# Kernel tuning notes

Hardware: AMD Instinct MI355X
Metric: run time of the kernel (lower is better)

## Reference

```python
import jax, jax.numpy as jnp
import numpy as np

B, S, HID = 1, 2048, 2048
H = 16
DN, DR, DV = 128, 64, 128          # qk_nope_head_dim, qk_rope_head_dim, v_head_dim
DQ = DN + DR                        # q_head_dim = 192
QLR, KVLR = 1536, 512               # q_lora_rank, kv_lora_rank
MAXP = 32 * 1024
SCALE = DQ ** -0.5
EPS = 1e-6


def rmsnorm(x, w):
    return x * jax.lax.rsqrt(jnp.mean(x * x, axis=-1, keepdims=True) + EPS) * w


def rotate_half(x):
    h = x.shape[-1] // 2
    return jnp.concatenate((-x[..., h:], x[..., :h]), axis=-1)


def interleave_to_half(x):
    # torch: view(b,h,s,d//2,2).transpose(4,3).reshape(b,h,s,d)
    b, h, s, d = x.shape
    return x.reshape(b, h, s, d // 2, 2).transpose(0, 1, 2, 4, 3).reshape(b, h, s, d)


def setup_inputs() -> dict:
    key = jax.random.key(0)
    ks = jax.random.split(key, 8)
    def w(k, shape):
        fan_in = shape[-1]
        return jax.random.normal(k, shape, jnp.float32) * (fan_in ** -0.5)
    inp = {
        "hidden_states": jax.random.normal(ks[0], (B, S, HID), jnp.float32),
        "q_a_w": w(ks[1], (QLR, HID)),
        "q_a_ln": jnp.ones((QLR,), jnp.float32),
        "q_b_w": w(ks[2], (H * DQ, QLR)),
        "kv_a_w": w(ks[3], (KVLR + DR, HID)),
        "kv_a_ln": jnp.ones((KVLR,), jnp.float32),
        "kv_b_w": w(ks[4], (H * (DN + DV), KVLR)),
        "o_w": w(ks[5], (HID, H * DV)),
    }
    # rotary tables, seq_len = 32k
    inv_freq = 1.0 / (10000.0 ** (np.arange(0, DR, 2, dtype=np.float32) / DR))
    t = np.arange(MAXP, dtype=np.float32)
    freqs = np.outer(t, inv_freq)
    emb = np.concatenate((freqs, freqs), axis=-1)
    inp["cos"] = jnp.asarray(np.cos(emb), jnp.float32)
    inp["sin"] = jnp.asarray(np.sin(emb), jnp.float32)
    # bool mask, True = masked (causal)
    inp["attention_mask"] = jnp.triu(jnp.ones((S, S), bool), 1)[None, None]
    inp["position_ids"] = jnp.arange(S, dtype=jnp.int64 if jax.config.jax_enable_x64 else jnp.int32)[None].repeat(B, 0)
    return inp


def reference(hidden_states, q_a_w, q_a_ln, q_b_w, kv_a_w, kv_a_ln, kv_b_w, o_w,
              cos, sin, attention_mask, position_ids):
    b, s, _ = hidden_states.shape
    # low-rank Q: q_b(LN(q_a(x)))
    q = rmsnorm(hidden_states @ q_a_w.T, q_a_ln) @ q_b_w.T         # [b,s,H*DQ]
    q = q.reshape(b, s, H, DQ).transpose(0, 2, 1, 3)               # [b,H,s,DQ]
    q_nope, q_pe = q[..., :DN], q[..., DN:]
    # compressed KV + decoupled rope key
    ckv = hidden_states @ kv_a_w.T                                  # [b,s,KVLR+DR]
    compressed_kv, k_pe = ckv[..., :KVLR], ckv[..., KVLR:]
    k_pe = k_pe.reshape(b, s, 1, DR).transpose(0, 2, 1, 3)          # [b,1,s,DR]
    kv = rmsnorm(compressed_kv, kv_a_ln) @ kv_b_w.T                 # [b,s,H*(DN+DV)]
    kv = kv.reshape(b, s, H, DN + DV).transpose(0, 2, 1, 3)         # [b,H,s,DN+DV]
    k_nope, value_states = kv[..., :DN], kv[..., DN:]
    # rotary with interleaved->half reorder on the rope slice only
    cos_p = cos[position_ids][:, None]                              # [b,1,s,DR]
    sin_p = sin[position_ids][:, None]
    q_pe = interleave_to_half(q_pe)
    k_pe = interleave_to_half(k_pe)
    q_pe = q_pe * cos_p + rotate_half(q_pe) * sin_p
    k_pe = k_pe * cos_p + rotate_half(k_pe) * sin_p
    query_states = jnp.concatenate((q_nope, q_pe), axis=-1)         # [b,H,s,DQ]
    key_states = jnp.concatenate(
        (k_nope, jnp.broadcast_to(k_pe, (b, H, s, DR))), axis=-1)   # [b,H,s,DQ]
    # manual attention
    scores = jnp.einsum("bhqd,bhkd->bhqk", query_states, key_states) * SCALE
    scores = jnp.where(attention_mask, jnp.float32(-10000.0), scores)
    attn = jax.nn.softmax(scores.astype(jnp.float32), axis=-1).astype(query_states.dtype)
    attn_out = jnp.einsum("bhqk,bhkd->bhqd", attn, value_states)    # [b,H,s,DV]
    attn_out = attn_out.transpose(0, 2, 1, 3).reshape(b, s, H * DV)
    return attn_out @ o_w.T                                         # [b,s,HID]
```

## Files before the change

kernel.cpp:

```cpp
#include <hip/hip_runtime.h>
#include <stdint.h>

typedef unsigned short u16;
typedef __attribute__((ext_vector_type(8))) short short8;
typedef __attribute__((ext_vector_type(4))) float f32x4;
typedef __attribute__((ext_vector_type(4))) unsigned short ushort4_t;
typedef __attribute__((ext_vector_type(4))) float float4_t;

#define DEV_INLINE __device__ __forceinline__

DEV_INLINE u16 f2bf(float f) {
    union { float f; unsigned u; } x; x.f = f;
    unsigned u = x.u;
    unsigned r = (u + 0x7FFFu + ((u >> 16) & 1u)) >> 16;
    return (u16)r;
}

DEV_INLINE float bf2f(u16 b) {
    union { unsigned u; float f; } x; x.u = ((unsigned)b) << 16;
    return x.f;
}

DEV_INLINE float fexp2(float x) {
    float r;
    asm("v_exp_f32 %0, %1" : "=v"(r) : "v"(x));
    return r;
}

DEV_INLINE unsigned cvtpk_bf16(float lo, float hi) {
    unsigned r;
    asm("v_cvt_pk_bf16_f32 %0, %1, %2" : "=v"(r) : "v"(lo), "v"(hi));
    return r;
}

template <int CTRL>
DEV_INLINE float dppmax(float x) {
    union { float f; int i; } u; u.f = x;
    int y = __builtin_amdgcn_update_dpp(u.i, u.i, CTRL, 0xf, 0xf, true);
    union { int i; float f; } v; v.i = y;
    return fmaxf(x, v.f);
}

DEV_INLINE float rmax16(float x) {
    x = dppmax<0xB1>(x);
    x = dppmax<0x4E>(x);
    x = dppmax<0x141>(x);
    x = dppmax<0x140>(x);
    return x;
}

__global__ void conv_multi(const float* __restrict__ s0, u16* __restrict__ d0, long e0,
                           const float* __restrict__ s1, u16* __restrict__ d1, long e1,
                           const float* __restrict__ s2, u16* __restrict__ d2, long e2,
                           const float* __restrict__ s3, u16* __restrict__ d3, long e3,
                           const float* __restrict__ s4, u16* __restrict__ d4, long e4) {
    long i = (long)blockIdx.x * 256 + threadIdx.x;
    const float* s; u16* d; long base;
    if      (i < e0) { s = s0; d = d0; base = 0; }
    else if (i < e1) { s = s1; d = d1; base = e0; }
    else if (i < e2) { s = s2; d = d2; base = e1; }
    else if (i < e3) { s = s3; d = d3; base = e2; }
    else if (i < e4) { s = s4; d = d4; base = e3; }
    else return;
    long j = i - base;
    float4_t v = ((const float4_t*)s)[j];
    ushort4_t o;
    o.x = f2bf(v.x); o.y = f2bf(v.y); o.z = f2bf(v.z); o.w = f2bf(v.w);
    ((ushort4_t*)d)[j] = o;
}

__global__ void conv_pad(const float* __restrict__ in, u16* __restrict__ out,
                         int rows_valid, long n4, int cols4) {
    long i = (long)blockIdx.x * blockDim.x + threadIdx.x;
    if (i >= n4) return;
    long row = i / cols4;
    ushort4_t o; o.x = 0; o.y = 0; o.z = 0; o.w = 0;
    if (row < rows_valid) {
        float4_t v = ((const float4_t*)in)[i];
        o.x = f2bf(v.x); o.y = f2bf(v.y); o.z = f2bf(v.z); o.w = f2bf(v.w);
    }
    ((ushort4_t*)out)[i] = o;
}

#define BK 32

DEV_INLINE void gload16(const u16* g, u16* l) {
    __builtin_amdgcn_global_load_lds((const __attribute__((address_space(1))) unsigned int*)g,
                                     (__attribute__((address_space(3))) unsigned int*)l,
                                     16, 0, 0);
}

template <typename OT>
__global__ __launch_bounds__(256) void gemm64_db(const u16* __restrict__ A, const u16* __restrict__ B,
                                                 OT* __restrict__ C, int M, int N, int K) {
    __shared__ u16 As[2][64 * BK];
    __shared__ u16 Bs[2][128 * BK];
    const int tid = threadIdx.x;
    const int wid = tid >> 6, lane = tid & 63;
    const int lm = lane & 15, lk = lane >> 4;
    const long bm = (long)blockIdx.y * 64, bn = (long)blockIdx.x * 128;

    f32x4 acc[4][2] = {};

    const int rowS = lane >> 2;
    const int colS = ((lane & 3) ^ ((lane >> 3) & 3)) * 8;
    const int cs = (lm >> 1) & 3;
    const u16* Ag = A + (bm + wid * 16 + rowS) * (long)K + colS;
    const u16* Bg = B + (bn + wid * 32 + rowS) * (long)K + colS;
    const int aoff = wid * 16 * BK;
    const int boff = wid * 32 * BK;

    gload16(Ag, &As[0][aoff]);
    gload16(Bg, &Bs[0][boff]);
    gload16(Bg + 16 * (long)K, &Bs[0][boff + 16 * BK]);
    __syncthreads();

    int cur = 0;
    for (int k0 = 0; k0 < K; k0 += BK) {
        if (k0 + BK < K) {
            gload16(Ag + k0 + BK, &As[cur ^ 1][aoff]);
            gload16(Bg + k0 + BK, &Bs[cur ^ 1][boff]);
            gload16(Bg + 16 * (long)K + k0 + BK, &Bs[cur ^ 1][boff + 16 * BK]);
        }
        short8 af[4], bfr[2];
#pragma unroll
        for (int m = 0; m < 4; ++m)
            af[m] = *(const short8*)&As[cur][(m * 16 + lm) * BK + (lk ^ cs) * 8];
#pragma unroll
        for (int n = 0; n < 2; ++n)
            bfr[n] = *(const short8*)&Bs[cur][(wid * 32 + n * 16 + lm) * BK + (lk ^ cs) * 8];
#pragma unroll
        for (int m = 0; m < 4; ++m)
#pragma unroll
            for (int n = 0; n < 2; ++n)
                acc[m][n] = __builtin_amdgcn_mfma_f32_16x16x32_bf16(af[m], bfr[n], acc[m][n], 0, 0, 0);
        __syncthreads();
        cur ^= 1;
    }

#pragma unroll
    for (int m = 0; m < 4; ++m)
#pragma unroll
        for (int n = 0; n < 2; ++n)
#pragma unroll
            for (int r = 0; r < 4; ++r) {
                long idx = (bm + m * 16 + lk * 4 + r) * (long)N + bn + wid * 32 + n * 16 + lm;
                if constexpr (sizeof(OT) == 4) C[idx] = acc[m][n][r];
                else                           C[idx] = f2bf(acc[m][n][r]);
            }
}

__global__ __launch_bounds__(256) void rmsnorm_bf16(const float* __restrict__ in, const float* __restrict__ w,
                                                    u16* __restrict__ out, int ldin, int ldout, int ncols) {
    const int row = blockIdx.x, tid = threadIdx.x;
    const float* x = in + (long)row * ldin;
    float ss = 0.f;
    for (int c = tid; c < ncols; c += 256) { float v = x[c]; ss = fmaf(v, v, ss); }
#pragma unroll
    for (int off = 32; off > 0; off >>= 1) ss += __shfl_down(ss, off);
    __shared__ float part[4];
    if ((tid & 63) == 0) part[tid >> 6] = ss;
    __syncthreads();
    float tot = part[0] + part[1] + part[2] + part[3];
    float rs = rsqrtf(tot / (float)ncols + 1e-6f);
    for (int c = tid; c < ncols; c += 256) out[(long)row * ldout + c] = f2bf(x[c] * rs * w[c]);
}

__global__ void rope_k(const float* __restrict__ ckv, const int* __restrict__ pos,
                       const float* __restrict__ cosT, const float* __restrict__ sinT,
                       u16* __restrict__ Kb) {
    int idx = blockIdx.x * 256 + threadIdx.x;
    if (idx >= 2048 * 32) return;
    int s = idx >> 5, j = idx & 31;
    long p = pos[s];
    const float* row = ckv + (long)s * 2176 + 2048;
    float x0 = row[2 * j], x1 = row[2 * j + 1];
    float c0 = cosT[p * 64 + j],      s0 = sinT[p * 64 + j];
    float c1 = cosT[p * 64 + 32 + j], s1 = sinT[p * 64 + 32 + j];
    u16 o0 = f2bf(x0 * c0 - x1 * s0);
    u16 o1 = f2bf(x1 * c1 + x0 * s1);
#pragma unroll
    for (int h = 0; h < 16; ++h) {
        u16* kr = Kb + ((long)h * 2048 + s) * 192 + 128;
        kr[j] = o0; kr[32 + j] = o1;
    }
}

__global__ void build_q(const u16* __restrict__ q, const int* __restrict__ pos,
                        const float* __restrict__ cosT, const float* __restrict__ sinT,
                        u16* __restrict__ Qb) {
    long idx = (long)blockIdx.x * 256 + threadIdx.x;
    if (idx >= 16L * 2048 * 192) return;
    int d = (int)(idx % 192);
    int s = (int)((idx / 192) % 2048);
    int h = (int)(idx / (192L * 2048));
    const u16* qrow = q + (long)s * 3072 + h * 192;
    u16 outv;
    if (d < 128) {
        outv = qrow[d];
    } else {
        long p = pos[s];
        int dd = d - 128;
        float cv = cosT[p * 64 + dd], sv = sinT[p * 64 + dd];
        float val;
        if (dd < 32) val = bf2f(qrow[128 + 2 * dd]) * cv - bf2f(qrow[128 + 2 * dd + 1]) * sv;
        else { int jj = dd - 32; val = bf2f(qrow[128 + 2 * jj + 1]) * cv + bf2f(qrow[128 + 2 * jj]) * sv; }
        outv = f2bf(val);
    }
    Qb[((long)h * 2048 + s) * 192 + d] = outv;
}

__global__ __launch_bounds__(256) void build_kv2(const u16* __restrict__ kv, u16* __restrict__ Kb,
                                                 u16* __restrict__ Vt) {
    __shared__ u16 Ls[128][72];
    const int h = blockIdx.y, s0 = blockIdx.x * 64;
    const int tid = threadIdx.x;
#pragma unroll
    for (int i = 0; i < 8; ++i) {
        int u = i * 256 + tid;
        int r = u >> 5, c8 = (u & 31) * 8;
        short8 x = *(const short8*)(kv + (long)(s0 + r) * 4096 + h * 256 + c8);
        if (c8 < 128) {
            *(short8*)(Kb + ((long)h * 2048 + s0 + r) * 192 + c8) = x;
        } else {
#pragma unroll
            for (int j = 0; j < 8; ++j) {
                int d = c8 - 128 + j;
                Ls[d][r ^ (((d >> 3) & 7) << 3)] = (u16)x[j];
            }
        }
    }
    __syncthreads();
#pragma unroll
    for (int i = 0; i < 8; ++i) {
        int u = i * 256 + tid;
        int d = u >> 4, s4 = (u & 15) * 4;
        int swz = ((d >> 3) & 7) << 3;
        ushort4_t v;
        v.x = Ls[d][(s4 + 0) ^ swz]; v.y = Ls[d][(s4 + 1) ^ swz];
        v.z = Ls[d][(s4 + 2) ^ swz]; v.w = Ls[d][(s4 + 3) ^ swz];
        *(ushort4_t*)(Vt + ((long)h * 128 + d) * 2048 + s0 + s4) = v;
    }
}

__global__ __launch_bounds__(512) void attn_fwd(const u16* __restrict__ Qb, const u16* __restrict__ Kb,
                                                const u16* __restrict__ Vt, u16* __restrict__ Ao) {
    __shared__ __align__(16) char smem[94720];

    const int b = blockIdx.x;
    const int h = (b & 7) * 2 + ((b >> 3) & 1);
    const int pi = b >> 4;
    const int tid = threadIdx.x;
    const int wid = tid >> 6, lane = tid & 63;
    const int lm = lane & 15, lk = lane >> 4;
    const int s = wid >> 2, wp = wid & 3;
    const int t256 = tid & 255;

    u16* Ks0 = (u16*)smem + s * 12800;
    u16* Vs0 = (u16*)(smem + 51200) + s * 8192;
    u16* PsW = (u16*)(smem + 83968) + wid * 640;
    float* ML = (float*)(smem + 94208);
    float* Ob = (float*)smem;

    const u16* Kh = Kb + (long)h * 2048 * 192;
    const u16* Vh = Vt + (long)h * 128 * 2048;

    short8 bones = {};
    if (lm == 0) {
#pragma unroll
        for (int j = 0; j < 8; ++j) bones[j] = (short)0x3F80;
    }
    const float C2 = 0.104117548f;

    for (int half = 0; half < 2; ++half) {
        const int qi = half ? (31 - pi) : pi;
        const int q0 = qi * 64;
        const int nt = 2 * qi + 2;
        const int niter = qi + 1;

        short8 qf[6];
        const u16* qbase = Qb + ((long)h * 2048 + q0 + wp * 16 + lm) * 192;
#pragma unroll
        for (int kf = 0; kf < 6; ++kf) qf[kf] = *(const short8*)(qbase + kf * 32 + lk * 8);

        f32x4 o[8] = {};
        f32x4 o9 = {};
        float mrow[4] = {-1e30f, -1e30f, -1e30f, -1e30f};

        short8 kreg[3], vreg[2];
        {
            const long k0 = s * 32;
#pragma unroll
            for (int i = 0; i < 3; ++i) {
                int idx = i * 256 + t256; int r = idx / 24, c = (idx % 24) * 8;
                kreg[i] = *(const short8*)(Kh + (k0 + r) * 192 + c);
            }
#pragma unroll
            for (int i = 0; i < 2; ++i) {
                int idx = i * 256 + t256; int dv = idx >> 2, kvb = idx & 3;
                vreg[i] = *(const short8*)(Vh + (long)dv * 2048 + k0 + kvb * 8);
            }
#pragma unroll
            for (int i = 0; i < 3; ++i) {
                int idx = i * 256 + t256; int r = idx / 24, c = (idx % 24) * 8;
                *(short8*)&Ks0[r * 200 + c] = kreg[i];
            }
#pragma unroll
            for (int i = 0; i < 2; ++i) {
                int idx = i * 256 + t256; int dv = idx >> 2, kvb = idx & 3;
                *(short8*)&Vs0[kvb * 1024 + ((dv * 8) ^ (kvb * 16))] = vreg[i];
            }
        }
        __syncthreads();

        int cur = 0;
        for (int it = 0; it < niter; ++it) {
            const int ts = 2 * it + s;
            const int k0 = ts * 32;
            const bool more = (it + 1 < niter);

            if (more) {
                const long k0n = (long)(ts + 2) * 32;
#pragma unroll
                for (int i = 0; i < 3; ++i) {
                    int idx = i * 256 + t256; int r = idx / 24, c = (idx % 24) * 8;
                    kreg[i] = *(const short8*)(Kh + (k0n + r) * 192 + c);
                }
#pragma unroll
                for (int i = 0; i < 2; ++i) {
                    int idx = i * 256 + t256; int dv = idx >> 2, kvb = idx & 3;
                    vreg[i] = *(const short8*)(Vh + (long)dv * 2048 + k0n + kvb * 8);
                }
            }

            const u16* KsC = Ks0 + cur * 6400;
            const u16* VsC = Vs0 + cur * 4096;

            f32x4 sfr[2] = {};
#pragma unroll
            for (int n = 0; n < 2; ++n)
#pragma unroll
                for (int kf = 0; kf < 6; ++kf) {
                    short8 kb = *(const short8*)&KsC[(n * 16 + lm) * 200 + kf * 32 + lk * 8];
                    sfr[n] = __builtin_amdgcn_mfma_f32_16x16x32_bf16(qf[kf], kb, sfr[n], 0, 0, 0);
                }

            float sv[2][4];
            const bool bt = (ts >= nt - 2);
#pragma unroll
            for (int n = 0; n < 2; ++n)
#pragma unroll
                for (int r = 0; r < 4; ++r) {
                    float val = sfr[n][r] * C2;
                    if (bt && (k0 + n * 16 + lm > q0 + wp * 16 + lk * 4 + r)) val = -1e30f;
                    sv[n][r] = val;
                }

            float pmax[4];
#pragma unroll
            for (int r = 0; r < 4; ++r)
                pmax[r] = rmax16(fmaxf(sv[0][r], sv[1][r]));
            bool need = (pmax[0] > mrow[0] + 8.f) || (pmax[1] > mrow[1] + 8.f) ||
                        (pmax[2] > mrow[2] + 8.f) || (pmax[3] > mrow[3] + 8.f);
            if (__any(need)) {
#pragma unroll
                for (int r = 0; r < 4; ++r) {
                    float mnew = fmaxf(mrow[r], pmax[r]);
                    float alpha = fexp2(mrow[r] - mnew);
                    mrow[r] = mnew;
#pragma unroll
                    for (int d = 0; d < 8; ++d) o[d][r] *= alpha;
                    o9[r] *= alpha;
                }
            }
#pragma unroll
            for (int n = 0; n < 2; ++n) {
                float p0 = fexp2(sv[n][0] - mrow[0]);
                float p1 = fexp2(sv[n][1] - mrow[1]);
                float p2 = fexp2(sv[n][2] - mrow[2]);
                float p3 = fexp2(sv[n][3] - mrow[3]);
                unsigned pk01 = cvtpk_bf16(p0, p1);
                unsigned pk23 = cvtpk_bf16(p2, p3);
                int rb = (lk * 4) * 40 + n * 16 + lm;
                PsW[rb]       = (u16)pk01;
                PsW[rb + 40]  = (u16)(pk01 >> 16);
                PsW[rb + 80]  = (u16)pk23;
                PsW[rb + 120] = (u16)(pk23 >> 16);
            }

            short8 pf = *(const short8*)&PsW[lm * 40 + lk * 8];
#pragma unroll
            for (int d = 0; d < 8; ++d) {
                short8 vf = *(const short8*)&VsC[lk * 1024 + (((d * 16 + lm) * 8) ^ (lk * 16))];
                o[d] = __builtin_amdgcn_mfma_f32_16x16x32_bf16(pf, vf, o[d], 0, 0, 0);
            }
            o9 = __builtin_amdgcn_mfma_f32_16x16x32_bf16(pf, bones, o9, 0, 0, 0);

            if (more) {
                u16* KsN = Ks0 + (cur ^ 1) * 6400;
                u16* VsN = Vs0 + (cur ^ 1) * 4096;
#pragma unroll
                for (int i = 0; i < 3; ++i) {
                    int idx = i * 256 + t256; int r = idx / 24, c = (idx % 24) * 8;
                    *(short8*)&KsN[r * 200 + c] = kreg[i];
                }
#pragma unroll
                for (int i = 0; i < 2; ++i) {
                    int idx = i * 256 + t256; int dv = idx >> 2, kvb = idx & 3;
                    *(short8*)&VsN[kvb * 1024 + ((dv * 8) ^ (kvb * 16))] = vreg[i];
                }
            }
            __syncthreads();
            cur ^= 1;
        }

        if (s == 1) {
#pragma unroll
            for (int d = 0; d < 8; ++d)
#pragma unroll
                for (int r = 0; r < 4; ++r)
                    Ob[(wp * 16 + lk * 4 + r) * 128 + d * 16 + lm] = o[d][r];
            if (lm == 0) {
#pragma unroll
                for (int r = 0; r < 4; ++r) {
                    int row = wp * 16 + lk * 4 + r;
                    ML[row * 2 + 0] = mrow[r];
                    ML[row * 2 + 1] = o9[r];
                }
            }
        }
        __syncthreads();
        if (s == 0) {
            float e0[4], e1[4], invl[4];
#pragma unroll
            for (int r = 0; r < 4; ++r) {
                int row = wp * 16 + lk * 4 + r;
                float m1 = ML[row * 2 + 0];
                float l1 = ML[row * 2 + 1];
                float l0 = __shfl(o9[r], lane & 48);
                float M = fmaxf(mrow[r], m1);
                e0[r] = fexp2(mrow[r] - M);
                e1[r] = fexp2(m1 - M);
                invl[r] = 1.f / (l0 * e0[r] + l1 * e1[r]);
            }
#pragma unroll
            for (int d = 0; d < 8; ++d)
#pragma unroll
                for (int r = 0; r < 4; ++r) {
                    int row = wp * 16 + lk * 4 + r;
                    float val = (o[d][r] * e0[r] +
                                 Ob[row * 128 + d * 16 + lm] * e1[r]) * invl[r];
                    Ao[((long)q0 + row) * 2048 + h * 128 + d * 16 + lm] = f2bf(val);
                }
        }
        __syncthreads();
    }
}

extern "C" void kernel_launch(void* const* d_in, const int* in_sizes, int n_in,
                              void* d_out, int out_size, void* d_ws, size_t ws_size,
                              hipStream_t stream) {
    (void)in_sizes; (void)n_in; (void)out_size; (void)ws_size;
    const float* hidden  = (const float*)d_in[0];
    const float* q_a_w   = (const float*)d_in[1];
    const float* q_a_ln  = (const float*)d_in[2];
    const float* q_b_w   = (const float*)d_in[3];
    const float* kv_a_w  = (const float*)d_in[4];
    const float* kv_a_ln = (const float*)d_in[5];
    const float* kv_b_w  = (const float*)d_in[6];
    const float* o_w     = (const float*)d_in[7];
    const float* cosT    = (const float*)d_in[8];
    const float* sinT    = (const float*)d_in[9];
    const int*   pos     = (const int*)d_in[11];

    char* ws = (char*)d_ws;
    u16* o_w_bf   = (u16*)(ws + 0);
    u16* qb_w_bf  = (u16*)(ws + 8388608);
    u16* kvb_w_bf = (u16*)(ws + 17825792);
    u16* qn_bf    = (u16*)(ws + 22020096);
    u16* kvn_bf   = (u16*)(ws + 28311552);
    u16* Qb       = (u16*)(ws + 30408704);
    u16* Kb       = (u16*)(ws + 42991616);
    u16* Vt       = (u16*)(ws + 55574528);
    u16* aout_bf  = (u16*)(ws + 63963136);
    u16*   hid_bf    = (u16*)(ws + 72351744);
    u16*   qkva_w_bf = (u16*)(ws + 80740352);
    float* qkva_f    = (float*)(ws + 89653248);
    u16*   q_f_bf    = (u16*)(ws + 72351744);
    u16*   kv_f_bf   = (u16*)(ws + 89653248);

    conv_multi<<<17920, 256, 0, stream>>>(
        hidden, hid_bf,    1048576L,
        q_a_w,  qkva_w_bf, 1835008L,
        q_b_w,  qb_w_bf,   3014656L,
        kv_b_w, kvb_w_bf,  3538944L,
        o_w,    o_w_bf,    4587520L);
    conv_pad<<<(640L*2048/4 + 255)/256, 256, 0, stream>>>(kv_a_w, qkva_w_bf + 1536L*2048, 576, 640L*2048/4, 512);

    gemm64_db<float><<<dim3(17, 32), 256, 0, stream>>>(hid_bf, qkva_w_bf, qkva_f, 2048, 2176, 2048);

    rmsnorm_bf16<<<2048, 256, 0, stream>>>(qkva_f, q_a_ln, qn_bf, 2176, 1536, 1536);
    rmsnorm_bf16<<<2048, 256, 0, stream>>>(qkva_f + 1536, kv_a_ln, kvn_bf, 2176, 512, 512);
    rope_k<<<(2048*32)/256, 256, 0, stream>>>(qkva_f, pos, cosT, sinT, Kb);

    gemm64_db<u16><<<dim3(24, 32), 256, 0, stream>>>(qn_bf, qb_w_bf, q_f_bf, 2048, 3072, 1536);
    gemm64_db<u16><<<dim3(32, 32), 256, 0, stream>>>(kvn_bf, kvb_w_bf, kv_f_bf, 2048, 4096, 512);

    build_q<<<(unsigned)((16L*2048*192 + 255)/256), 256, 0, stream>>>(q_f_bf, pos, cosT, sinT, Qb);
    build_kv2<<<dim3(32, 16), 256, 0, stream>>>(kv_f_bf, Kb, Vt);

    attn_fwd<<<256, 512, 0, stream>>>(Qb, Kb, Vt, aout_bf);

    gemm64_db<float><<<dim3(16, 32), 256, 0, stream>>>(aout_bf, o_w_bf, (float*)d_out, 2048, 2048, 2048);
}
```

Baseline: 246.2 us.

## Triple-buffer GEMM loads with vmcnt waits and XOR-swizzle attention K tile

The GEMM moves from a double-buffered loop to a three-stage LDS pipeline. It prefetches two K-tiles ahead and replaces __syncthreads with explicit vmcnt waits plus s_barrier, so global-to-LDS loads overlap more MFMA work. The attention kernel drops the padded 200-element K row stride for a dense 192 stride with an XOR swizzle on 16-byte chunks. This avoids LDS bank conflicts without padding and shrinks shared memory. The triple buffer raises GEMM LDS use, and the hand-written waitcnt logic must match the number of outstanding loads.

```diff
diff --git a/kernel.cpp b/kernel.cpp
--- a/kernel.cpp
+++ b/kernel.cpp
@@ -91,10 +91,10 @@
 }
 
 template <typename OT>
-__global__ __launch_bounds__(256) void gemm64_db(const u16* __restrict__ A, const u16* __restrict__ B,
+__global__ __launch_bounds__(256) void gemm64_p3(const u16* __restrict__ A, const u16* __restrict__ B,
                                                  OT* __restrict__ C, int M, int N, int K) {
-    __shared__ u16 As[2][64 * BK];
-    __shared__ u16 Bs[2][128 * BK];
+    __shared__ u16 As[3][64 * BK];
+    __shared__ u16 Bs[3][128 * BK];
     const int tid = threadIdx.x;
     const int wid = tid >> 6, lane = tid & 63;
     const int lm = lane & 15, lk = lane >> 4;
@@ -110,17 +110,27 @@
     const int aoff = wid * 16 * BK;
     const int boff = wid * 32 * BK;
 
-    gload16(Ag, &As[0][aoff]);
-    gload16(Bg, &Bs[0][boff]);
-    gload16(Bg + 16 * (long)K, &Bs[0][boff + 16 * BK]);
-    __syncthreads();
-
-    int cur = 0;
-    for (int k0 = 0; k0 < K; k0 += BK) {
-        if (k0 + BK < K) {
-            gload16(Ag + k0 + BK, &As[cur ^ 1][aoff]);
-            gload16(Bg + k0 + BK, &Bs[cur ^ 1][boff]);
-            gload16(Bg + 16 * (long)K + k0 + BK, &Bs[cur ^ 1][boff + 16 * BK]);
+    const int nst = K / BK;
+
+#define STAGE(kk, bb)                                                             \
+    do {                                                                          \
+        gload16(Ag + (kk) * BK, &As[bb][aoff]);                                   \
+        gload16(Bg + (kk) * BK, &Bs[bb][boff]);                                   \
+        gload16(Bg + 16 * (long)K + (kk) * BK, &Bs[bb][boff + 16 * BK]);          \
+    } while (0)
+
+    STAGE(0, 0);
+    STAGE(1, 1);
+    asm volatile("s_waitcnt vmcnt(3)" ::: "memory");
+    __builtin_amdgcn_s_barrier();
+    asm volatile("" ::: "memory");
+
+    for (int k = 0; k < nst; ++k) {
+        const int cur = k % 3;
+        const bool more = (k + 2 < nst);
+        if (more) {
+            const int nb = (k + 2) % 3;
+            STAGE(k + 2, nb);
         }
         short8 af[4], bfr[2];
 #pragma unroll
@@ -134,9 +144,12 @@
 #pragma unroll
             for (int n = 0; n < 2; ++n)
                 acc[m][n] = __builtin_amdgcn_mfma_f32_16x16x32_bf16(af[m], bfr[n], acc[m][n], 0, 0, 0);
-        __syncthreads();
-        cur ^= 1;
-    }
+        if (more) asm volatile("s_waitcnt vmcnt(3)" ::: "memory");
+        else      asm volatile("s_waitcnt vmcnt(0)" ::: "memory");
+        __builtin_amdgcn_s_barrier();
+        asm volatile("" ::: "memory");
+    }
+#undef STAGE
 
 #pragma unroll
     for (int m = 0; m < 4; ++m)
@@ -245,7 +258,7 @@
 
 __global__ __launch_bounds__(512) void attn_fwd(const u16* __restrict__ Qb, const u16* __restrict__ Kb,
                                                 const u16* __restrict__ Vt, u16* __restrict__ Ao) {
-    __shared__ __align__(16) char smem[94720];
+    __shared__ __align__(16) char smem[92672];
 
     const int b = blockIdx.x;
     const int h = (b & 7) * 2 + ((b >> 3) & 1);
@@ -256,10 +269,10 @@
     const int s = wid >> 2, wp = wid & 3;
     const int t256 = tid & 255;
 
-    u16* Ks0 = (u16*)smem + s * 12800;
-    u16* Vs0 = (u16*)(smem + 51200) + s * 8192;
-    u16* PsW = (u16*)(smem + 83968) + wid * 640;
-    float* ML = (float*)(smem + 94208);
+    u16* Ks0 = (u16*)smem + s * 12288;
+    u16* Vs0 = (u16*)(smem + 49152) + s * 8192;
+    u16* PsW = (u16*)(smem + 81920) + wid * 640;
+    float* ML = (float*)(smem + 92160);
     float* Ob = (float*)smem;
 
     const u16* Kh = Kb + (long)h * 2048 * 192;
@@ -302,8 +315,8 @@
             }
 #pragma unroll
             for (int i = 0; i < 3; ++i) {
-                int idx = i * 256 + t256; int r = idx / 24, c = (idx % 24) * 8;
-                *(short8*)&Ks0[r * 200 + c] = kreg[i];
+                int idx = i * 256 + t256; int r = idx / 24, c8 = idx % 24;
+                *(short8*)&Ks0[r * 192 + ((c8 ^ (r & 7)) << 3)] = kreg[i];
             }
 #pragma unroll
             for (int i = 0; i < 2; ++i) {
@@ -333,7 +346,7 @@
                 }
             }
 
-            const u16* KsC = Ks0 + cur * 6400;
+            const u16* KsC = Ks0 + cur * 6144;
             const u16* VsC = Vs0 + cur * 4096;
 
             f32x4 sfr[2] = {};
@@ -341,7 +354,7 @@
             for (int n = 0; n < 2; ++n)
 #pragma unroll
                 for (int kf = 0; kf < 6; ++kf) {
-                    short8 kb = *(const short8*)&KsC[(n * 16 + lm) * 200 + kf * 32 + lk * 8];
+                    short8 kb = *(const short8*)&KsC[(n * 16 + lm) * 192 + (((kf * 4 + lk) ^ (lm & 7)) << 3)];
                     sfr[n] = __builtin_amdgcn_mfma_f32_16x16x32_bf16(qf[kf], kb, sfr[n], 0, 0, 0);
                 }
 
@@ -397,12 +410,12 @@
             o9 = __builtin_amdgcn_mfma_f32_16x16x32_bf16(pf, bones, o9, 0, 0, 0);
 
             if (more) {
-                u16* KsN = Ks0 + (cur ^ 1) * 6400;
+                u16* KsN = Ks0 + (cur ^ 1) * 6144;
                 u16* VsN = Vs0 + (cur ^ 1) * 4096;
 #pragma unroll
                 for (int i = 0; i < 3; ++i) {
-                    int idx = i * 256 + t256; int r = idx / 24, c = (idx % 24) * 8;
-                    *(short8*)&KsN[r * 200 + c] = kreg[i];
+                    int idx = i * 256 + t256; int r = idx / 24, c8 = idx % 24;
+                    *(short8*)&KsN[r * 192 + ((c8 ^ (r & 7)) << 3)] = kreg[i];
                 }
 #pragma unroll
                 for (int i = 0; i < 2; ++i) {
@@ -497,19 +510,19 @@
         o_w,    o_w_bf,    4587520L);
     conv_pad<<<(640L*2048/4 + 255)/256, 256, 0, stream>>>(kv_a_w, qkva_w_bf + 1536L*2048, 576, 640L*2048/4, 512);
 
-    gemm64_db<float><<<dim3(17, 32), 256, 0, stream>>>(hid_bf, qkva_w_bf, qkva_f, 2048, 2176, 2048);
+    gemm64_p3<float><<<dim3(17, 32), 256, 0, stream>>>(hid_bf, qkva_w_bf, qkva_f, 2048, 2176, 2048);
 
     rmsnorm_bf16<<<2048, 256, 0, stream>>>(qkva_f, q_a_ln, qn_bf, 2176, 1536, 1536);
     rmsnorm_bf16<<<2048, 256, 0, stream>>>(qkva_f + 1536, kv_a_ln, kvn_bf, 2176, 512, 512);
     rope_k<<<(2048*32)/256, 256, 0, stream>>>(qkva_f, pos, cosT, sinT, Kb);
 
-    gemm64_db<u16><<<dim3(24, 32), 256, 0, stream>>>(qn_bf, qb_w_bf, q_f_bf, 2048, 3072, 1536);
-    gemm64_db<u16><<<dim3(32, 32), 256, 0, stream>>>(kvn_bf, kvb_w_bf, kv_f_bf, 2048, 4096, 512);
+    gemm64_p3<u16><<<dim3(24, 32), 256, 0, stream>>>(qn_bf, qb_w_bf, q_f_bf, 2048, 3072, 1536);
+    gemm64_p3<u16><<<dim3(32, 32), 256, 0, stream>>>(kvn_bf, kvb_w_bf, kv_f_bf, 2048, 4096, 512);
 
     build_q<<<(unsigned)((16L*2048*192 + 255)/256), 256, 0, stream>>>(q_f_bf, pos, cosT, sinT, Qb);
     build_kv2<<<dim3(32, 16), 256, 0, stream>>>(kv_f_bf, Kb, Vt);
 
     attn_fwd<<<256, 512, 0, stream>>>(Qb, Kb, Vt, aout_bf);
 
-    gemm64_db<float><<<dim3(16, 32), 256, 0, stream>>>(aout_bf, o_w_bf, (float*)d_out, 2048, 2048, 2048);
-}
+    gemm64_p3<float><<<dim3(16, 32), 256, 0, stream>>>(aout_bf, o_w_bf, (float*)d_out, 2048, 2048, 2048);
+}
```

Result: slower. 253.3 us (+2.9%).
